# Kernel optimization log

Hardware: AMD Instinct MI355X
Metric: run time of the kernel (lower is better)

The kernel has to match this reference:

```python
import jax, jax.numpy as jnp
import numpy as np

B, S, D, H = 2, 2048, 1024, 16
DK = D // H
NEG = -1e9


def setup_inputs() -> dict:
    key = jax.random.key(0)
    ks = jax.random.split(key, 11)
    s = 1.0 / np.sqrt(D)
    inp = {
        "q": jax.random.normal(ks[0], (B, S, D), jnp.float32),
        "k": jax.random.normal(ks[1], (B, S, D), jnp.float32),
        "v": jax.random.normal(ks[2], (B, S, D), jnp.float32),
        "mask": jnp.tril(jnp.ones((S, S), jnp.int32))[None, None],  # [1,1,S,S] causal
        "Wq": jax.random.normal(ks[3], (D, D), jnp.float32) * s,
        "bq": jnp.zeros((D,), jnp.float32),
        "Wk": jax.random.normal(ks[4], (D, D), jnp.float32) * s,
        "bk": jnp.zeros((D,), jnp.float32),
        "Wv": jax.random.normal(ks[5], (D, D), jnp.float32) * s,
        "bv": jnp.zeros((D,), jnp.float32),
        "Wo": jax.random.normal(ks[6], (D, D), jnp.float32) * s,
        "bo": jnp.zeros((D,), jnp.float32),
    }
    return inp


def reference(q, k, v, mask, Wq, bq, Wk, bk, Wv, bv, Wo, bo):
    # projections (torch Linear: x @ W.T + b)
    Q = q @ Wq.T + bq
    K = k @ Wk.T + bk
    V = v @ Wv.T + bv
    # [B,S,D] -> [B,H,S,DK]
    Q = Q.reshape(B, S, H, DK).transpose(0, 2, 1, 3)
    K = K.reshape(B, S, H, DK).transpose(0, 2, 1, 3)
    V = V.reshape(B, S, H, DK).transpose(0, 2, 1, 3)
    scores = jnp.einsum("bhqd,bhkd->bhqk", Q, K) / jnp.sqrt(jnp.float32(DK))
    scores = jnp.where(mask == 0, jnp.float32(NEG), scores)
    attn = jax.nn.softmax(scores, axis=-1)  # dropout p=0.0 -> identity
    x = jnp.einsum("bhqk,bhkd->bhqd", attn, V)
    x = x.transpose(0, 2, 1, 3).reshape(B, S, D)
    return x @ Wo.T + bo
```

## Files before the change

### kernel.cpp

```cpp
#include <hip/hip_runtime.h>
#include <hip/hip_bf16.h>


typedef __bf16 bf16_t;
typedef __bf16 bf16x4 __attribute__((ext_vector_type(4)));
typedef __bf16 bf16x8 __attribute__((ext_vector_type(8)));
typedef float f32x4 __attribute__((ext_vector_type(4)));

#define BB 2
#define SS 2048
#define DD 1024
#define HH 16
#define DKK 64
#define MM 4096

#define NELT ((size_t)BB * SS * DD)
#define WELT ((size_t)DD * DD)

__device__ __align__(16) bf16_t g_ws[7 * NELT + 4 * WELT];

__device__ __forceinline__ void gld16(const bf16_t* g, bf16_t* l) {
    __builtin_amdgcn_global_load_lds(
        (const __attribute__((address_space(1))) void*)g,
        (__attribute__((address_space(3))) void*)l, 16, 0, 0);
}

__global__ __launch_bounds__(256) void cvt7(
    const float* __restrict__ q,  const float* __restrict__ k,  const float* __restrict__ v,
    const float* __restrict__ Wq, const float* __restrict__ Wk, const float* __restrict__ Wv,
    const float* __restrict__ Wo,
    bf16_t* __restrict__ qb, bf16_t* __restrict__ kb, bf16_t* __restrict__ vb,
    bf16_t* __restrict__ Wqb, bf16_t* __restrict__ Wkb, bf16_t* __restrict__ Wvb,
    bf16_t* __restrict__ Wob)
{
    const float* s; bf16_t* d; size_t n;
    switch (blockIdx.y) {
        case 0: s = q;  d = qb;  n = NELT; break;
        case 1: s = k;  d = kb;  n = NELT; break;
        case 2: s = v;  d = vb;  n = NELT; break;
        case 3: s = Wq; d = Wqb; n = WELT; break;
        case 4: s = Wk; d = Wkb; n = WELT; break;
        case 5: s = Wv; d = Wvb; n = WELT; break;
        default: s = Wo; d = Wob; n = WELT; break;
    }
    size_t e = ((size_t)blockIdx.x * 256 + threadIdx.x) * 8;
    if (e >= n) return;
    f32x4 a = *(const f32x4*)(s + e);
    f32x4 b = *(const f32x4*)(s + e + 4);
    bf16x8 o;
    #pragma unroll
    for (int i = 0; i < 4; ++i) { o[i] = (bf16_t)a[i]; o[4 + i] = (bf16_t)b[i]; }
    *(bf16x8*)(d + e) = o;
}

#define BM 128
#define BN 128
#define BKG 64
#define LDC 136

__global__ __launch_bounds__(256) void gemm_qkv3(
    const bf16_t* __restrict__ qb, const bf16_t* __restrict__ kb, const bf16_t* __restrict__ vb,
    const bf16_t* __restrict__ Wqb, const bf16_t* __restrict__ Wkb, const bf16_t* __restrict__ Wvb,
    const float* __restrict__ bq, const float* __restrict__ bk, const float* __restrict__ bv,
    bf16_t* __restrict__ Qp, bf16_t* __restrict__ Kp, bf16_t* __restrict__ Vt)
{
    const int z = blockIdx.z;
    const bf16_t* A    = (z == 0) ? qb  : (z == 1) ? kb  : vb;
    const bf16_t* W    = (z == 0) ? Wqb : (z == 1) ? Wkb : Wvb;
    const float*  bias = (z == 0) ? bq  : (z == 1) ? bk  : bv;

    __shared__ __align__(16) bf16_t smem[128 * LDC];
    bf16_t (*As)[BKG] = (bf16_t(*)[BKG])smem;
    bf16_t (*Bs)[BKG] = (bf16_t(*)[BKG])(smem + 128 * BKG);
    bf16_t (*Ct)[LDC] = (bf16_t(*)[LDC])smem;

    const int tid  = threadIdx.x;
    const int wave = tid >> 6;
    const int lane = tid & 63;
    const int quad = lane >> 4;
    const int c16  = lane & 15;
    const int bm = blockIdx.x * BM;
    const int bn = blockIdx.y * BN;
    const int wm = (wave >> 1) * 64;
    const int wn = (wave & 1) * 64;

    const int srow = lane >> 3;
    const int scol = (lane & 7) * 8;

    f32x4 acc[4][4] = {};

    for (int k0 = 0; k0 < DD; k0 += BKG) {
        __syncthreads();
        #pragma unroll
        for (int j = 0; j < 4; ++j) {
            int r0 = wave * 32 + j * 8;
            gld16(A + (size_t)(bm + r0 + srow) * DD + k0 + scol, &As[r0][0]);
            gld16(W + (size_t)(bn + r0 + srow) * DD + k0 + scol, &Bs[r0][0]);
        }
        __syncthreads();

        #pragma unroll
        for (int ks = 0; ks < 2; ++ks) {
            bf16x8 af[4], bfr[4];
            #pragma unroll
            for (int tm = 0; tm < 4; ++tm)
                af[tm] = *(const bf16x8*)(&As[wm + tm * 16 + c16][ks * 32 + quad * 8]);
            #pragma unroll
            for (int tn = 0; tn < 4; ++tn)
                bfr[tn] = *(const bf16x8*)(&Bs[wn + tn * 16 + c16][ks * 32 + quad * 8]);
            #pragma unroll
            for (int tm = 0; tm < 4; ++tm)
                #pragma unroll
                for (int tn = 0; tn < 4; ++tn)
                    acc[tm][tn] = __builtin_amdgcn_mfma_f32_16x16x32_bf16(
                        af[tm], bfr[tn], acc[tm][tn], 0, 0, 0);
        }
    }

    float bia[4];
    #pragma unroll
    for (int tn = 0; tn < 4; ++tn)
        bia[tn] = bias[bn + wn + tn * 16 + c16];

    if (z < 2) {
        const float osc = (z == 0) ? 0.125f : 1.0f;
        bf16_t* C = (z == 0) ? Qp : Kp;
        #pragma unroll
        for (int tm = 0; tm < 4; ++tm)
            #pragma unroll
            for (int r = 0; r < 4; ++r) {
                size_t base = (size_t)(bm + wm + tm * 16 + quad * 4 + r) * DD;
                #pragma unroll
                for (int tn = 0; tn < 4; ++tn)
                    C[base + bn + wn + tn * 16 + c16] =
                        (bf16_t)((acc[tm][tn][r] + bia[tn]) * osc);
            }
    } else {
        __syncthreads();
        #pragma unroll
        for (int tm = 0; tm < 4; ++tm)
            #pragma unroll
            for (int tn = 0; tn < 4; ++tn) {
                bf16x4 pk;
                #pragma unroll
                for (int r = 0; r < 4; ++r)
                    pk[r] = (bf16_t)(acc[tm][tn][r] + bia[tn]);
                *(bf16x4*)(&Ct[wn + tn * 16 + c16][wm + tm * 16 + quad * 4]) = pk;
            }
        __syncthreads();
        const int b_    = bm >> 11;
        const int sbase = bm & (SS - 1);
        #pragma unroll
        for (int p = 0; p < 4; ++p) {
            int col = p * 32 + (tid >> 3);
            int si  = (tid & 7) * 8;
            size_t rowoff = (size_t)(b_ * 1024 + bn + col) * SS + sbase;
            #pragma unroll
            for (int half = 0; half < 2; ++half) {
                int s = si + half * 64;
                *(bf16x8*)(&Vt[rowoff + s]) = *(const bf16x8*)(&Ct[col][s]);
            }
        }
    }
}

__global__ __launch_bounds__(256) void gemm_out(
    const bf16_t* __restrict__ A,
    const bf16_t* __restrict__ W,
    const float* __restrict__ bias,
    float* __restrict__ C)
{
    __shared__ __align__(16) bf16_t As[128][BKG];
    __shared__ __align__(16) bf16_t Bs[64][BKG];

    const int tid  = threadIdx.x;
    const int wave = tid >> 6;
    const int lane = tid & 63;
    const int quad = lane >> 4;
    const int c16  = lane & 15;
    const int bm = blockIdx.x * 128;
    const int bn = blockIdx.y * 64;
    const int wm = (wave >> 1) * 64;
    const int wn = (wave & 1) * 32;

    const int srow = lane >> 3;
    const int scol = (lane & 7) * 8;

    f32x4 acc[4][2] = {};

    for (int k0 = 0; k0 < DD; k0 += BKG) {
        __syncthreads();
        #pragma unroll
        for (int j = 0; j < 4; ++j) {
            int r0 = wave * 32 + j * 8;
            gld16(A + (size_t)(bm + r0 + srow) * DD + k0 + scol, &As[r0][0]);
        }
        #pragma unroll
        for (int j = 0; j < 2; ++j) {
            int r0 = wave * 16 + j * 8;
            gld16(W + (size_t)(bn + r0 + srow) * DD + k0 + scol, &Bs[r0][0]);
        }
        __syncthreads();

        #pragma unroll
        for (int ks = 0; ks < 2; ++ks) {
            bf16x8 af[4], bfr[2];
            #pragma unroll
            for (int tm = 0; tm < 4; ++tm)
                af[tm] = *(const bf16x8*)(&As[wm + tm * 16 + c16][ks * 32 + quad * 8]);
            #pragma unroll
            for (int tn = 0; tn < 2; ++tn)
                bfr[tn] = *(const bf16x8*)(&Bs[wn + tn * 16 + c16][ks * 32 + quad * 8]);
            #pragma unroll
            for (int tm = 0; tm < 4; ++tm)
                #pragma unroll
                for (int tn = 0; tn < 2; ++tn)
                    acc[tm][tn] = __builtin_amdgcn_mfma_f32_16x16x32_bf16(
                        af[tm], bfr[tn], acc[tm][tn], 0, 0, 0);
        }
    }

    float bia[2];
    #pragma unroll
    for (int tn = 0; tn < 2; ++tn)
        bia[tn] = bias[bn + wn + tn * 16 + c16];

    #pragma unroll
    for (int tm = 0; tm < 4; ++tm)
        #pragma unroll
        for (int r = 0; r < 4; ++r) {
            size_t base = (size_t)(bm + wm + tm * 16 + quad * 4 + r) * DD;
            #pragma unroll
            for (int tn = 0; tn < 2; ++tn)
                C[base + bn + wn + tn * 16 + c16] = acc[tm][tn][r] + bia[tn];
        }
}

#define LDPS 40
#define LDCF 68
#define PSLOT (4 * 32 * LDPS)

#define LOADK(KF, UU)                                                          \
do {                                                                           \
    const int kb_ = (UU) * 32;                                                 \
    const bf16_t* kp0 = Kb + (size_t)(kb_ + c16) * DD;                         \
    const bf16_t* kp1 = Kb + (size_t)(kb_ + 16 + c16) * DD;                    \
    KF[0][0] = *(const bf16x8*)(kp0 + quad * 8);                               \
    KF[0][1] = *(const bf16x8*)(kp0 + 32 + quad * 8);                          \
    KF[1][0] = *(const bf16x8*)(kp1 + quad * 8);                               \
    KF[1][1] = *(const bf16x8*)(kp1 + 32 + quad * 8);                          \
} while (0)

#define ATTN_STEP(UU, KFC, KFN, VFC, VFP, PW, PR, DOPV)                        \
do {                                                                           \
    const int kb_ = (UU) * 32;                                                 \
    f32x4 sc_[2][2];                                                           \
    _Pragma("unroll")                                                          \
    for (int tm = 0; tm < 2; ++tm)                                             \
        _Pragma("unroll")                                                      \
        for (int ct = 0; ct < 2; ++ct) {                                       \
            f32x4 s_ = {};                                                     \
            s_ = __builtin_amdgcn_mfma_f32_16x16x32_bf16(                      \
                     KFC[ct][0], qf[tm][0], s_, 0, 0, 0);                      \
            s_ = __builtin_amdgcn_mfma_f32_16x16x32_bf16(                      \
                     KFC[ct][1], qf[tm][1], s_, 0, 0, 0);                      \
            sc_[tm][ct] = s_;                                                  \
        }                                                                      \
    if ((UU) + 4 < U) LOADK(KFN, (UU) + 4);                                    \
    _Pragma("unroll")                                                          \
    for (int tn = 0; tn < 4; ++tn)                                             \
        VFC[tn] = *(const bf16x8*)(Vb + (size_t)(tn * 16 + c16) * SS           \
                                   + kb_ + quad * 8);                          \
    const bool needmask_ = (kb_ == qbase);                                     \
    bf16x4 w_[2][2];                                                           \
    _Pragma("unroll")                                                          \
    for (int tm = 0; tm < 2; ++tm) {                                           \
        const int qrow_ = qbase + tm * 16 + c16;                               \
        _Pragma("unroll")                                                      \
        for (int ct = 0; ct < 2; ++ct)                                         \
            _Pragma("unroll")                                                  \
            for (int r = 0; r < 4; ++r) {                                      \
                float s_ = sc_[tm][ct][r];                                     \
                if (needmask_ && (kb_ + ct * 16 + quad * 4 + r > qrow_))       \
                    s_ = -1e9f;                                                \
                float p_ = __expf(s_);                                         \
                lsum2[tm] += p_;                                               \
                w_[tm][ct][r] = (bf16_t)p_;                                    \
            }                                                                  \
    }                                                                          \
    if (DOPV) {                                                                \
        _Pragma("unroll")                                                      \
        for (int tm = 0; tm < 2; ++tm) {                                       \
            bf16x8 pa_ = *(const bf16x8*)((PR) + tm * 16 * LDPS);              \
            _Pragma("unroll")                                                  \
            for (int tn = 0; tn < 4; ++tn)                                     \
                oacc[tm][tn] = __builtin_amdgcn_mfma_f32_16x16x32_bf16(        \
                    pa_, VFP[tn], oacc[tm][tn], 0, 0, 0);                      \
        }                                                                      \
    }                                                                          \
    _Pragma("unroll")                                                          \
    for (int tm = 0; tm < 2; ++tm)                                             \
        _Pragma("unroll")                                                      \
        for (int ct = 0; ct < 2; ++ct)                                         \
            *(bf16x4*)((PW) + tm * 16 * LDPS + ct * 16) = w_[tm][ct];          \
} while (0)

#define PVFIN(PR, VFP)                                                         \
do {                                                                           \
    _Pragma("unroll")                                                          \
    for (int tm = 0; tm < 2; ++tm) {                                           \
        bf16x8 pa_ = *(const bf16x8*)((PR) + tm * 16 * LDPS);                  \
        _Pragma("unroll")                                                      \
        for (int tn = 0; tn < 4; ++tn)                                         \
            oacc[tm][tn] = __builtin_amdgcn_mfma_f32_16x16x32_bf16(            \
                pa_, VFP[tn], oacc[tm][tn], 0, 0, 0);                          \
    }                                                                          \
} while (0)

__global__ __launch_bounds__(256) void attn_fwd9(
    const bf16_t* __restrict__ Q,
    const bf16_t* __restrict__ K,
    const bf16_t* __restrict__ Vt,
    bf16_t* __restrict__ O)
{
    const int flat = blockIdx.x;
    const int bh   = (flat & 7) * 4 + (flat >> 8);
    const int pair = (flat >> 3) & 31;
    const int b = bh >> 4;
    const int h = bh & 15;

    const int wave = threadIdx.x >> 6;
    const int lane = threadIdx.x & 63;
    const int quad = lane >> 4;
    const int c16  = lane & 15;

    __shared__ __align__(16) unsigned char smraw[2 * PSLOT * 2];
    bf16_t (*Ps)[4][32][LDPS] = (bf16_t(*)[4][32][LDPS])smraw;
    float  (*Cf)[16][LDCF]    = (float(*)[16][LDCF])smraw;
    __shared__ float Ls[4][32];

    const bf16_t* Kb = K  + (size_t)b * SS * DD + h * DKK;
    const bf16_t* Vb = Vt + (size_t)(b * 1024 + h * DKK) * SS;

    bf16_t*       pw0 = &Ps[0][wave][c16][quad * 4];
    const bf16_t* pr0 = &Ps[0][wave][c16][quad * 8];
    bf16_t*       pw1 = pw0 + PSLOT;
    const bf16_t* pr1 = pr0 + PSLOT;

    for (int t = 0; t < 2; ++t) {
        const int qt    = (t == 0) ? (63 - pair) : pair;
        const int qbase = qt * 32;
        const int U     = qt + 1;

        bf16x8 qf[2][2];
        #pragma unroll
        for (int tm = 0; tm < 2; ++tm) {
            const bf16_t* qp = Q + ((size_t)b * SS + qbase + tm * 16 + c16) * DD + h * DKK;
            qf[tm][0] = *(const bf16x8*)(qp + quad * 8);
            qf[tm][1] = *(const bf16x8*)(qp + 32 + quad * 8);
        }

        f32x4 oacc[2][4] = {};
        float lsum2[2] = {0.f, 0.f};

        bf16x8 kfA[2][2], kfB[2][2];
        bf16x8 vfA[4], vfB[4];

        {
            int u = wave;
            if (u < U) {
                LOADK(kfA, u);
                ATTN_STEP(u, kfA, kfB, vfA, vfB, pw0, pr1, 0);
                u += 4;
                for (;;) {
                    if (u >= U) { PVFIN(pr0, vfA); break; }
                    ATTN_STEP(u, kfB, kfA, vfB, vfA, pw1, pr0, 1);
                    u += 4;
                    if (u >= U) { PVFIN(pr1, vfB); break; }
                    ATTN_STEP(u, kfA, kfB, vfA, vfB, pw0, pr1, 1);
                    u += 4;
                }
            }
        }

        #pragma unroll
        for (int tm = 0; tm < 2; ++tm) {
            float l = lsum2[tm];
            l += __shfl_xor(l, 16, 64);
            l += __shfl_xor(l, 32, 64);
            if (lane < 16) Ls[wave][tm * 16 + lane] = l;
        }

        const int row = threadIdx.x >> 4;
        const int col = (threadIdx.x & 15) * 4;
        #pragma unroll
        for (int tm = 0; tm < 2; ++tm) {
            __syncthreads();
            #pragma unroll
            for (int tn = 0; tn < 4; ++tn)
                #pragma unroll
                for (int r = 0; r < 4; ++r)
                    Cf[wave][quad * 4 + r][tn * 16 + c16] = oacc[tm][tn][r];
            __syncthreads();
            f32x4 ssum = {};
            #pragma unroll
            for (int p = 0; p < 4; ++p)
                ssum += *(const f32x4*)(&Cf[p][row][col]);
            float l = Ls[0][tm * 16 + row] + Ls[1][tm * 16 + row]
                    + Ls[2][tm * 16 + row] + Ls[3][tm * 16 + row];
            float inv = 1.0f / l;
            bf16x4 o;
            #pragma unroll
            for (int i = 0; i < 4; ++i) o[i] = (bf16_t)(ssum[i] * inv);
            *(bf16x4*)(&O[((size_t)b * SS + qbase + tm * 16 + row) * DD + h * DKK + col]) = o;
        }
        __syncthreads();
    }
}

extern "C" void kernel_launch(void* const* d_in, const int* in_sizes, int n_in,
                              void* d_out, int out_size, void* d_ws, size_t ws_size,
                              hipStream_t stream) {
    (void)in_sizes; (void)n_in; (void)out_size; (void)d_ws; (void)ws_size;
    const float* q  = (const float*)d_in[0];
    const float* k  = (const float*)d_in[1];
    const float* v  = (const float*)d_in[2];
    const float* Wq = (const float*)d_in[4];
    const float* bq = (const float*)d_in[5];
    const float* Wk = (const float*)d_in[6];
    const float* bk = (const float*)d_in[7];
    const float* Wv = (const float*)d_in[8];
    const float* bv = (const float*)d_in[9];
    const float* Wo = (const float*)d_in[10];
    const float* bo = (const float*)d_in[11];

    bf16_t* ws;
    hipGetSymbolAddress((void**)&ws, HIP_SYMBOL(g_ws));
    bf16_t* Qp  = ws;
    bf16_t* Kp  = Qp + NELT;
    bf16_t* Vt  = Kp + NELT;
    bf16_t* Xa  = Vt + NELT;
    bf16_t* qb  = Xa + NELT;
    bf16_t* kb  = qb + NELT;
    bf16_t* vb  = kb + NELT;
    bf16_t* Wqb = vb + NELT;
    bf16_t* Wkb = Wqb + WELT;
    bf16_t* Wvb = Wkb + WELT;
    bf16_t* Wob = Wvb + WELT;

    cvt7<<<dim3(2048, 7), 256, 0, stream>>>(q, k, v, Wq, Wk, Wv, Wo,
                                            qb, kb, vb, Wqb, Wkb, Wvb, Wob);

    gemm_qkv3<<<dim3(MM / BM, DD / BN, 3), 256, 0, stream>>>(
        qb, kb, vb, Wqb, Wkb, Wvb, bq, bk, bv, Qp, Kp, Vt);

    attn_fwd9<<<dim3(1024), 256, 0, stream>>>(Qp, Kp, Vt, Xa);

    gemm_out<<<dim3(MM / 128, DD / 64), 256, 0, stream>>>(Xa, Wob, bo, (float*)d_out);
}
```

Measured before the change: 285.6 us.

## Fold log2e into Q scale, use exp2, drop P double-buffer, add setprio

The log2(e) factor is folded into the Q projection scale so the attention softmax can use the native exp2 instruction instead of expf. The software-pipelined attention step, which double-buffered P in LDS and deferred the PV matmul by one iteration, is replaced by a simpler step that writes P, waits on LDS, and does the PV MFMAs right away. s_setprio raises wave priority around the MFMA sections. This cuts LDS use and register pressure, at the cost of losing the overlap between the PV MFMAs and the next step's softmax work.

New measurement: 275.4 us. 3.6% less time.

```diff
diff --git a/kernel.cpp b/kernel.cpp
--- a/kernel.cpp
+++ b/kernel.cpp
@@ -123,7 +123,7 @@
         bia[tn] = bias[bn + wn + tn * 16 + c16];
 
     if (z < 2) {
-        const float osc = (z == 0) ? 0.125f : 1.0f;
+        const float osc = (z == 0) ? 0.125f * 1.4426950408889634f : 1.0f;
         bf16_t* C = (z == 0) ? Qp : Kp;
         #pragma unroll
         for (int tm = 0; tm < 4; ++tm)
@@ -238,7 +238,6 @@
 
 #define LDPS 40
 #define LDCF 68
-#define PSLOT (4 * 32 * LDPS)
 
 #define LOADK(KF, UU)                                                          \
 do {                                                                           \
@@ -251,10 +250,11 @@
     KF[1][1] = *(const bf16x8*)(kp1 + 32 + quad * 8);                          \
 } while (0)
 
-#define ATTN_STEP(UU, KFC, KFN, VFC, VFP, PW, PR, DOPV)                        \
+#define ATTN_STEP(UU, KFC, KFN)                                                \
 do {                                                                           \
     const int kb_ = (UU) * 32;                                                 \
     f32x4 sc_[2][2];                                                           \
+    __builtin_amdgcn_s_setprio(1);                                             \
     _Pragma("unroll")                                                          \
     for (int tm = 0; tm < 2; ++tm)                                             \
         _Pragma("unroll")                                                      \
@@ -266,58 +266,46 @@
                      KFC[ct][1], qf[tm][1], s_, 0, 0, 0);                      \
             sc_[tm][ct] = s_;                                                  \
         }                                                                      \
+    __builtin_amdgcn_s_setprio(0);                                             \
     if ((UU) + 4 < U) LOADK(KFN, (UU) + 4);                                    \
+    bf16x8 vf_[4];                                                             \
     _Pragma("unroll")                                                          \
     for (int tn = 0; tn < 4; ++tn)                                             \
-        VFC[tn] = *(const bf16x8*)(Vb + (size_t)(tn * 16 + c16) * SS           \
+        vf_[tn] = *(const bf16x8*)(Vb + (size_t)(tn * 16 + c16) * SS           \
                                    + kb_ + quad * 8);                          \
     const bool needmask_ = (kb_ == qbase);                                     \
-    bf16x4 w_[2][2];                                                           \
     _Pragma("unroll")                                                          \
     for (int tm = 0; tm < 2; ++tm) {                                           \
         const int qrow_ = qbase + tm * 16 + c16;                               \
         _Pragma("unroll")                                                      \
-        for (int ct = 0; ct < 2; ++ct)                                         \
+        for (int ct = 0; ct < 2; ++ct) {                                       \
+            bf16x4 w_;                                                         \
             _Pragma("unroll")                                                  \
             for (int r = 0; r < 4; ++r) {                                      \
                 float s_ = sc_[tm][ct][r];                                     \
                 if (needmask_ && (kb_ + ct * 16 + quad * 4 + r > qrow_))       \
                     s_ = -1e9f;                                                \
-                float p_ = __expf(s_);                                         \
+                float p_ = __builtin_amdgcn_exp2f(s_);                         \
                 lsum2[tm] += p_;                                               \
-                w_[tm][ct][r] = (bf16_t)p_;                                    \
+                w_[r] = (bf16_t)p_;                                            \
             }                                                                  \
-    }                                                                          \
-    if (DOPV) {                                                                \
-        _Pragma("unroll")                                                      \
-        for (int tm = 0; tm < 2; ++tm) {                                       \
-            bf16x8 pa_ = *(const bf16x8*)((PR) + tm * 16 * LDPS);              \
-            _Pragma("unroll")                                                  \
-            for (int tn = 0; tn < 4; ++tn)                                     \
-                oacc[tm][tn] = __builtin_amdgcn_mfma_f32_16x16x32_bf16(        \
-                    pa_, VFP[tn], oacc[tm][tn], 0, 0, 0);                      \
+            *(bf16x4*)(pw + tm * 16 * LDPS + ct * 16) = w_;                    \
         }                                                                      \
     }                                                                          \
-    _Pragma("unroll")                                                          \
-    for (int tm = 0; tm < 2; ++tm)                                             \
-        _Pragma("unroll")                                                      \
-        for (int ct = 0; ct < 2; ++ct)                                         \
-            *(bf16x4*)((PW) + tm * 16 * LDPS + ct * 16) = w_[tm][ct];          \
-} while (0)
-
-#define PVFIN(PR, VFP)                                                         \
-do {                                                                           \
+    asm volatile("s_waitcnt lgkmcnt(0)" ::: "memory");                         \
+    __builtin_amdgcn_s_setprio(1);                                             \
     _Pragma("unroll")                                                          \
     for (int tm = 0; tm < 2; ++tm) {                                           \
-        bf16x8 pa_ = *(const bf16x8*)((PR) + tm * 16 * LDPS);                  \
+        bf16x8 pa_ = *(const bf16x8*)(pr + tm * 16 * LDPS);                    \
         _Pragma("unroll")                                                      \
         for (int tn = 0; tn < 4; ++tn)                                         \
             oacc[tm][tn] = __builtin_amdgcn_mfma_f32_16x16x32_bf16(            \
-                pa_, VFP[tn], oacc[tm][tn], 0, 0, 0);                          \
+                pa_, vf_[tn], oacc[tm][tn], 0, 0, 0);                          \
     }                                                                          \
+    __builtin_amdgcn_s_setprio(0);                                             \
 } while (0)
 
-__global__ __launch_bounds__(256) void attn_fwd9(
+__global__ __launch_bounds__(256) void attn_fwd11(
     const bf16_t* __restrict__ Q,
     const bf16_t* __restrict__ K,
     const bf16_t* __restrict__ Vt,
@@ -334,18 +322,16 @@
     const int quad = lane >> 4;
     const int c16  = lane & 15;
 
-    __shared__ __align__(16) unsigned char smraw[2 * PSLOT * 2];
-    bf16_t (*Ps)[4][32][LDPS] = (bf16_t(*)[4][32][LDPS])smraw;
-    float  (*Cf)[16][LDCF]    = (float(*)[16][LDCF])smraw;
+    __shared__ __align__(16) unsigned char smraw[4 * 16 * LDCF * 4];
+    bf16_t (*Ps)[32][LDPS] = (bf16_t(*)[32][LDPS])smraw;
+    float  (*Cf)[16][LDCF] = (float(*)[16][LDCF])smraw;
     __shared__ float Ls[4][32];
 
     const bf16_t* Kb = K  + (size_t)b * SS * DD + h * DKK;
     const bf16_t* Vb = Vt + (size_t)(b * 1024 + h * DKK) * SS;
 
-    bf16_t*       pw0 = &Ps[0][wave][c16][quad * 4];
-    const bf16_t* pr0 = &Ps[0][wave][c16][quad * 8];
-    bf16_t*       pw1 = pw0 + PSLOT;
-    const bf16_t* pr1 = pr0 + PSLOT;
+    bf16_t*       pw = &Ps[wave][c16][quad * 4];
+    const bf16_t* pr = &Ps[wave][c16][quad * 8];
 
     for (int t = 0; t < 2; ++t) {
         const int qt    = (t == 0) ? (63 - pair) : pair;
@@ -364,21 +350,16 @@
         float lsum2[2] = {0.f, 0.f};
 
         bf16x8 kfA[2][2], kfB[2][2];
-        bf16x8 vfA[4], vfB[4];
 
         {
             int u = wave;
             if (u < U) {
                 LOADK(kfA, u);
-                ATTN_STEP(u, kfA, kfB, vfA, vfB, pw0, pr1, 0);
-                u += 4;
                 for (;;) {
-                    if (u >= U) { PVFIN(pr0, vfA); break; }
-                    ATTN_STEP(u, kfB, kfA, vfB, vfA, pw1, pr0, 1);
-                    u += 4;
-                    if (u >= U) { PVFIN(pr1, vfB); break; }
-                    ATTN_STEP(u, kfA, kfB, vfA, vfB, pw0, pr1, 1);
-                    u += 4;
+                    ATTN_STEP(u, kfA, kfB); u += 4;
+                    if (u >= U) break;
+                    ATTN_STEP(u, kfB, kfA); u += 4;
+                    if (u >= U) break;
                 }
             }
         }
@@ -454,7 +435,7 @@
     gemm_qkv3<<<dim3(MM / BM, DD / BN, 3), 256, 0, stream>>>(
         qb, kb, vb, Wqb, Wkb, Wvb, bq, bk, bv, Qp, Kp, Vt);
 
-    attn_fwd9<<<dim3(1024), 256, 0, stream>>>(Qp, Kp, Vt, Xa);
+    attn_fwd11<<<dim3(1024), 256, 0, stream>>>(Qp, Kp, Vt, Xa);
 
     gemm_out<<<dim3(MM / 128, DD / 64), 256, 0, stream>>>(Xa, Wob, bo, (float*)d_out);
 }
```
